# Kernel tuning notes

Measured on AMD Instinct MI355X. Metric: run time of the kernel, lower is better.

## Reference

```python
import jax, jax.numpy as jnp
import numpy as np

NUM_HEADS = 8
HEAD_DIM = 64
AVG_K_LENGTH = 20
SCALE = 1.0 / (HEAD_DIM ** 0.5 * float(np.log(AVG_K_LENGTH)))  # 1/(sqrt(dim)*log(avg_k_length))


def setup_inputs() -> dict:
    key = jax.random.key(0)
    k1, k2, k3, k4 = jax.random.split(key, 4)
    B, HD, LQ, LK = 4, NUM_HEADS * HEAD_DIM, 2048, 2048
    q = jax.random.normal(k1, (B, HD, LQ), dtype=jnp.float32)
    k = jax.random.normal(k2, (B, HD, LK), dtype=jnp.float32)
    v = jax.random.normal(k3, (B, HD, LK), dtype=jnp.float32)
    k_length = jax.random.randint(k4, (B,), 512, LK + 1, dtype=jnp.int32)
    return {"q": q, "k": k, "v": v, "k_length": k_length}


def reference(q, k, v, k_length):
    b, hd, lq = q.shape
    lk = k.shape[-1]
    d = hd // NUM_HEADS
    # b (h d) l -> b h d l
    qh = q.reshape(b, NUM_HEADS, d, lq)
    kh = k.reshape(b, NUM_HEADS, d, lk)
    vh = v.reshape(b, NUM_HEADS, d, lk)
    # per-batch entropy-invariance scale: scale * log(k_length)
    s = SCALE * jnp.log(k_length.astype(jnp.float32))[:, None, None, None]  # (b,1,1,1)
    attn = jnp.einsum('bhdq,bhdk->bhqk', qh, kh)  # (b,h,lq,lk)
    attn = jax.nn.softmax(s * attn, axis=-1)
    out = jnp.einsum('bhqk,bhdk->bhdq', attn, vh)  # (b,h,d,lq)
    return out.reshape(b, hd, lq)
```

## Files before the change

### kernel.cpp

```cpp
#include <hip/hip_runtime.h>
#include <hip/hip_bf16.h>
#include <math.h>


typedef __attribute__((ext_vector_type(8))) short short8_t;
typedef __attribute__((ext_vector_type(4))) short short4_t;
typedef __attribute__((ext_vector_type(4))) float float4_t;

#define SEQ   2048
#define NBH   32
#define NKT   32

__device__ __forceinline__ unsigned f2bf2u(float a, float b) {
#if __has_builtin(__builtin_amdgcn_cvt_pk_bf16_f32)
  typedef __bf16 bf16x2_t __attribute__((ext_vector_type(2)));
  union { bf16x2_t v; unsigned u; } cv;
  cv.v = __builtin_amdgcn_cvt_pk_bf16_f32(a, b);
  return cv.u;
#else
  union { float f; unsigned u; } x, y;
  x.f = a; y.f = b;
  unsigned ra = x.u + 0x7fffu + ((x.u >> 16) & 1u);
  unsigned rb = y.u + 0x7fffu + ((y.u >> 16) & 1u);
  return (ra >> 16) | (rb & 0xffff0000u);
#endif
}

__device__ __forceinline__ short f2bf1(float a) {
  return (short)(f2bf2u(a, a) & 0xffffu);
}

__device__ __forceinline__ float fast_exp2(float x) {
#if __has_builtin(__builtin_amdgcn_exp2f)
  return __builtin_amdgcn_exp2f(x);
#else
  return exp2f(x);
#endif
}

__device__ __forceinline__ void gld16(const void* g, void* l) {
  __builtin_amdgcn_global_load_lds(
      (const __attribute__((address_space(1))) void*)g,
      (__attribute__((address_space(3))) void*)l, 16, 0, 0);
}

__device__ __forceinline__ float4_t mfma32(short8_t a, short8_t b, float4_t c) {
  return __builtin_amdgcn_mfma_f32_16x16x32_bf16(a, b, c, 0, 0, 0);
}

__device__ __forceinline__ float4_t mfma16(short4_t a, short4_t b, float4_t c) {
#if __has_builtin(__builtin_amdgcn_mfma_f32_16x16x16bf16_1k)
  return __builtin_amdgcn_mfma_f32_16x16x16bf16_1k(a, b, c, 0, 0, 0);
#else
  asm("v_mfma_f32_16x16x16_bf16 %0, %1, %2, %0" : "+v"(c) : "v"(a), "v"(b));
  return c;
#endif
}

#define PST 68
__global__ __launch_bounds__(256, 8)
void eia_prep_kernel(const float* __restrict__ kg, const float* __restrict__ vg,
                     unsigned short* __restrict__ Kt2, unsigned short* __restrict__ Vt2) {
  __shared__ __align__(16) short T[64 * PST];
  const int id  = blockIdx.x;
  const int isV = id >> 10;
  const int sub = id & 1023;
  const int bh  = sub >> 5;
  const int kt  = sub & 31;
  const int t   = threadIdx.x;

  if (!isV) {
    const size_t ib = ((size_t)bh * 64) * SEQ + (size_t)(kt * 64) + (t & 63);
    const int dg = t >> 6;
#pragma unroll
    for (int dd = 0; dd < 16; dd += 4) {
      const int d = dg * 16 + dd;
      const float f0 = kg[ib + (size_t)(d + 0) * SEQ];
      const float f1 = kg[ib + (size_t)(d + 1) * SEQ];
      const float f2 = kg[ib + (size_t)(d + 2) * SEQ];
      const float f3 = kg[ib + (size_t)(d + 3) * SEQ];
      union { short4_t s; unsigned u[2]; } p;
      p.u[0] = f2bf2u(f0, f1);
      p.u[1] = f2bf2u(f2, f3);
      *(short4_t*)&T[(t & 63) * PST + d] = p.s;
    }
    __syncthreads();
    unsigned short* outt = Kt2 + (size_t)(bh * 32 + kt) * 4096;
#pragma unroll
    for (int rep = 0; rep < 2; ++rep) {
      const int id2 = rep * 256 + t;
      const int lr = id2 & 63, ch = id2 >> 6;
      union { short8_t v; short4_t h[2]; } o;
      o.h[0] = *(const short4_t*)&T[lr * PST + ch * 8];
      o.h[1] = *(const short4_t*)&T[lr * PST + ch * 8 + 4];
      *(short8_t*)&outt[ch * 512 + lr * 8] = o.v;
    }
  } else {
#pragma unroll
    for (int rep = 0; rep < 4; ++rep) {
      const int id2 = rep * 256 + t;
      const int d = id2 >> 4, l4 = (id2 & 15) * 4;
      const float4_t f = *(const float4_t*)&vg[((size_t)bh * 64 + d) * SEQ + kt * 64 + l4];
      union { short4_t s; unsigned u[2]; } p;
      p.u[0] = f2bf2u(f[0], f[1]);
      p.u[1] = f2bf2u(f[2], f[3]);
      *(short4_t*)&T[d * PST + l4] = p.s;
    }
    __syncthreads();
    unsigned short* outt = Vt2 + (size_t)(bh * 32 + kt) * 4096;
#pragma unroll
    for (int rep = 0; rep < 2; ++rep) {
      const int c = rep * 256 + t;
      const int k4 = c >> 5, dp = c & 31;
      union { short8_t v; short4_t h[2]; } o;
      o.h[0] = *(const short4_t*)&T[(2 * dp) * PST + k4 * 4];
      o.h[1] = *(const short4_t*)&T[(2 * dp + 1) * PST + k4 * 4];
      *(short8_t*)&outt[k4 * 256 + dp * 8] = o.v;
    }
  }
}

__global__ __launch_bounds__(256, 2)
void eia_attn_kernel(const float* __restrict__ qg,
                     const unsigned short* __restrict__ Kt2,
                     const unsigned short* __restrict__ Vt2,
                     const int* __restrict__ klen,
                     float* __restrict__ outg) {
  __shared__ __align__(16) short SM[24576];

  const int tid  = threadIdx.x;
  const int bh   = blockIdx.x & 31;
  const int qt   = blockIdx.x >> 5;
  const int q0   = qt * 128;
  const int w    = tid >> 6;
  const int lane = tid & 63;
  const int quad = lane >> 4;
  const int l16  = lane & 15;

  const float c = (1.4426950408889634f / (8.0f * 2.9957322735539909f)) *
                  logf((float)klen[bh >> 3]);
  const size_t qb = (size_t)bh * 64 * SEQ;

#pragma unroll
  for (int rep = 0; rep < 8; ++rep) {
    const int id = rep * 256 + tid;
    const int d  = id >> 5;
    const int q4 = (id & 31) * 4;
    const float4_t f = *(const float4_t*)&qg[qb + (size_t)d * SEQ + (size_t)(q0 + q4)];
    SM[(q4 + 0) * 68 + d] = f2bf1(c * f[0]);
    SM[(q4 + 1) * 68 + d] = f2bf1(c * f[1]);
    SM[(q4 + 2) * 68 + d] = f2bf1(c * f[2]);
    SM[(q4 + 3) * 68 + d] = f2bf1(c * f[3]);
  }
  __syncthreads();

  short8_t qfrag[2][2];
#pragma unroll
  for (int g = 0; g < 2; ++g)
#pragma unroll
    for (int s = 0; s < 2; ++s) {
      const short* qp = &SM[(w * 32 + g * 16 + l16) * 68 + s * 32 + quad * 8];
      const short4_t lo = *(const short4_t*)qp;
      const short4_t hi = *(const short4_t*)(qp + 4);
      qfrag[g][s] = short8_t{lo[0], lo[1], lo[2], lo[3], hi[0], hi[1], hi[2], hi[3]};
    }
  __syncthreads();

  const char* ksrc = (const char*)Kt2 + (size_t)bh * NKT * 8192 + (2 * w) * 1024 + lane * 16;
  const char* vsrc = (const char*)Vt2 + (size_t)bh * NKT * 8192 + (2 * w) * 1024 + lane * 16;
  short* const kdst = &SM[(2 * w) * 512];
  short* const vdst = &SM[12288 + (2 * w) * 512];

  const short* const kfp = &SM[quad * 512 + l16 * 8];
  const short* const vfp = &SM[12288 + quad * 256 + l16 * 4];

  const float4_t z4 = {0.f, 0.f, 0.f, 0.f};
  float4_t oacc[2][4];
#pragma unroll
  for (int g = 0; g < 2; ++g)
#pragma unroll
    for (int tt = 0; tt < 4; ++tt) oacc[g][tt] = z4;
  float4_t lacc[2] = {z4, z4};
  const short one_bf = (short)0x3F80;
  const short4_t ones4 = (l16 == 0) ? short4_t{one_bf, one_bf, one_bf, one_bf}
                                    : short4_t{0, 0, 0, 0};

  gld16(ksrc, kdst);              gld16(ksrc + 1024, kdst + 512);
  gld16(vsrc, vdst);              gld16(vsrc + 1024, vdst + 512);
  gld16(ksrc + 8192, kdst + 4096); gld16(ksrc + 8192 + 1024, kdst + 4096 + 512);
  gld16(vsrc + 8192, vdst + 4096); gld16(vsrc + 8192 + 1024, vdst + 4096 + 512);

  int  sc = 0;
  int  sn = 2;
  size_t gsrc = 2 * 8192;

  for (int kt = 0; kt < NKT; ++kt) {
    if (kt < NKT - 1) asm volatile("s_waitcnt vmcnt(4)" ::: "memory");
    else              asm volatile("s_waitcnt vmcnt(0)" ::: "memory");
    asm volatile("s_barrier" ::: "memory");

    if (kt < NKT - 2) {
      const int so = sn * 4096;
      gld16(ksrc + gsrc, kdst + so); gld16(ksrc + gsrc + 1024, kdst + so + 512);
      gld16(vsrc + gsrc, vdst + so); gld16(vsrc + gsrc + 1024, vdst + so + 512);
      gsrc += 8192;
      sn = (sn == 2) ? 0 : sn + 1;
    }
    const int koff = sc * 4096;
    sc = (sc == 2) ? 0 : sc + 1;
    const short* const kb = kfp + koff;
    const short* const vb = vfp + koff;

    float4_t sac[2][4];
#pragma unroll
    for (int t = 0; t < 4; ++t) {
      const short8_t kv = *(const short8_t*)(kb + t * 128);
      sac[0][t] = mfma32(kv, qfrag[0][0], z4);
      sac[1][t] = mfma32(kv, qfrag[1][0], z4);
    }
#pragma unroll
    for (int t = 0; t < 4; ++t) {
      const short8_t kv = *(const short8_t*)(kb + 2048 + t * 128);
      sac[0][t] = mfma32(kv, qfrag[0][1], sac[0][t]);
      sac[1][t] = mfma32(kv, qfrag[1][1], sac[1][t]);
    }

    short4_t pbf[2][4];
#pragma unroll
    for (int g = 0; g < 2; ++g)
#pragma unroll
      for (int t = 0; t < 4; ++t) {
        const float e0 = fast_exp2(sac[g][t][0]);
        const float e1 = fast_exp2(sac[g][t][1]);
        const float e2 = fast_exp2(sac[g][t][2]);
        const float e3 = fast_exp2(sac[g][t][3]);
        union { short4_t s; unsigned u[2]; } p;
        p.u[0] = f2bf2u(e0, e1);
        p.u[1] = f2bf2u(e2, e3);
        pbf[g][t] = p.s;
        lacc[g] = mfma16(ones4, pbf[g][t], lacc[g]);
      }

#pragma unroll
    for (int t = 0; t < 4; ++t) {
      const short* vfb = vb + t * 1024;
#pragma unroll
      for (int tt = 0; tt < 4; ++tt) {
        const short4_t vv = *(const short4_t*)(vfb + tt * 64);
        oacc[0][tt] = mfma16(vv, pbf[0][t], oacc[0][tt]);
        oacc[1][tt] = mfma16(vv, pbf[1][t], oacc[1][tt]);
      }
    }
  }

#pragma unroll
  for (int g = 0; g < 2; ++g) {
    const float ls  = __shfl(lacc[g][0], l16, 64);
    const float inv = 1.0f / ls;
    const size_t ob = qb + (size_t)(q0 + w * 32 + g * 16 + l16);
#pragma unroll
    for (int tt = 0; tt < 4; ++tt)
#pragma unroll
      for (int r = 0; r < 4; ++r)
        outg[ob + (size_t)(tt * 16 + quad * 4 + r) * SEQ] = oacc[g][tt][r] * inv;
  }
}

#define DPAD  72
#define PPAD  68
__global__ __launch_bounds__(256, 5)
void eia_attn_fb(const float* __restrict__ qg, const float* __restrict__ kg,
                 const float* __restrict__ vg, const int* __restrict__ klen,
                 float* __restrict__ outg) {
  __shared__ __align__(16) short QPs[64 * DPAD];
  __shared__ __align__(16) short Ksf[64 * DPAD];
  __shared__ __align__(16) short Vsf[64 * DPAD];

  const int tid  = threadIdx.x;
  const int bh   = blockIdx.x & 31;
  const int qt   = blockIdx.x >> 5;
  const int q0   = qt * 64;
  const int w    = tid >> 6;
  const int lane = tid & 63;
  const int quad = lane >> 4;
  const int l16  = lane & 15;

  const size_t base = (size_t)bh * 64 * SEQ;
  const float c = (1.4426950408889634f / (8.0f * 2.9957322735539909f)) *
                  logf((float)klen[bh >> 3]);

#pragma unroll
  for (int it = 0; it < 2; ++it) {
    const int e = it * 4 + w;
    float f[8];
#pragma unroll
    for (int j = 0; j < 8; ++j)
      f[j] = c * qg[base + (size_t)(e * 8 + j) * SEQ + (size_t)(q0 + lane)];
    union { short8_t s8; unsigned u[4]; } t;
#pragma unroll
    for (int j = 0; j < 4; ++j) t.u[j] = f2bf2u(f[2 * j], f[2 * j + 1]);
    *(short8_t*)&QPs[lane * DPAD + e * 8] = t.s8;
  }
  __syncthreads();

  short8_t qfrag[2];
#pragma unroll
  for (int s = 0; s < 2; ++s)
    qfrag[s] = *(const short8_t*)&QPs[(w * 16 + l16) * DPAD + s * 32 + quad * 8];

  float4_t oacc[4];
#pragma unroll
  for (int t = 0; t < 4; ++t) { oacc[t][0] = 0.f; oacc[t][1] = 0.f; oacc[t][2] = 0.f; oacc[t][3] = 0.f; }
  float lsumv[4] = {0.f, 0.f, 0.f, 0.f};
  const int pbase = w * (16 * DPAD);

  for (int kt = 0; kt < NKT; ++kt) {
    const int k0 = kt * 64;
#pragma unroll
    for (int it = 0; it < 2; ++it) {
      float f[8];
#pragma unroll
      for (int j = 0; j < 8; ++j)
        f[j] = kg[base + (size_t)((it * 4 + w) * 8 + j) * SEQ + (size_t)(k0 + lane)];
      union { short8_t s8; unsigned u[4]; } t;
#pragma unroll
      for (int j = 0; j < 4; ++j) t.u[j] = f2bf2u(f[2 * j], f[2 * j + 1]);
      *(short8_t*)&Ksf[lane * DPAD + (it * 4 + w) * 8] = t.s8;
    }
#pragma unroll
    for (int it = 0; it < 4; ++it) {
      const int d = it * 16 + (w << 2) + (lane >> 4);
      const float4_t vv = *(const float4_t*)&vg[base + (size_t)d * SEQ + (size_t)(k0 + ((lane & 15) << 2))];
      union { short4_t s4; unsigned u[2]; } t;
      t.u[0] = f2bf2u(vv[0], vv[1]);
      t.u[1] = f2bf2u(vv[2], vv[3]);
      *(short4_t*)&Vsf[d * DPAD + ((lane & 15) << 2)] = t.s4;
    }
    __syncthreads();

    float4_t sacc[4];
#pragma unroll
    for (int t = 0; t < 4; ++t) { sacc[t][0] = 0.f; sacc[t][1] = 0.f; sacc[t][2] = 0.f; sacc[t][3] = 0.f; }
#pragma unroll
    for (int t = 0; t < 4; ++t)
#pragma unroll
      for (int s = 0; s < 2; ++s) {
        const short8_t bf = *(const short8_t*)&Ksf[(t * 16 + l16) * DPAD + s * 32 + quad * 8];
        sacc[t] = mfma32(qfrag[s], bf, sacc[t]);
      }

#pragma unroll
    for (int r = 0; r < 4; ++r) {
      const float p0 = fast_exp2(sacc[0][r]);
      const float p1 = fast_exp2(sacc[1][r]);
      const float p2 = fast_exp2(sacc[2][r]);
      const float p3 = fast_exp2(sacc[3][r]);
      lsumv[r] += (p0 + p1) + (p2 + p3);
      const int prow = pbase + (quad * 4 + r) * PPAD + l16;
      QPs[prow +  0] = f2bf1(p0);
      QPs[prow + 16] = f2bf1(p1);
      QPs[prow + 32] = f2bf1(p2);
      QPs[prow + 48] = f2bf1(p3);
    }

#pragma unroll
    for (int s = 0; s < 2; ++s) {
      const short* pr = &QPs[pbase + l16 * PPAD + s * 32 + quad * 8];
      const short4_t plo = *(const short4_t*)pr;
      const short4_t phi = *(const short4_t*)(pr + 4);
      const short8_t pf = {plo[0], plo[1], plo[2], plo[3], phi[0], phi[1], phi[2], phi[3]};
#pragma unroll
      for (int t = 0; t < 4; ++t) {
        const short8_t vf = *(const short8_t*)&Vsf[(t * 16 + l16) * DPAD + s * 32 + quad * 8];
        oacc[t] = mfma32(pf, vf, oacc[t]);
      }
    }
    __syncthreads();
  }

  float inv[4];
#pragma unroll
  for (int r = 0; r < 4; ++r) {
    float v = lsumv[r];
    v += __shfl_xor(v, 1);
    v += __shfl_xor(v, 2);
    v += __shfl_xor(v, 4);
    v += __shfl_xor(v, 8);
    inv[r] = 1.0f / v;
  }
#pragma unroll
  for (int t = 0; t < 4; ++t)
#pragma unroll
    for (int r = 0; r < 4; ++r)
      outg[base + (size_t)(t * 16 + l16) * SEQ +
           (size_t)(q0 + w * 16 + quad * 4 + r)] = oacc[t][r] * inv[r];
}

extern "C" void kernel_launch(void* const* d_in, const int* in_sizes, int n_in,
                              void* d_out, int out_size, void* d_ws, size_t ws_size,
                              hipStream_t stream) {
  const float* q  = (const float*)d_in[0];
  const float* k  = (const float*)d_in[1];
  const float* v  = (const float*)d_in[2];
  const int*   kl = (const int*)d_in[3];
  float* out = (float*)d_out;

  const size_t TEN  = (size_t)NBH * SEQ * 64;
  const size_t need = 2 * TEN * sizeof(unsigned short);

  if (ws_size >= need) {
    unsigned short* Kt2 = (unsigned short*)d_ws;
    unsigned short* Vt2 = Kt2 + TEN;
    eia_prep_kernel<<<2048, 256, 0, stream>>>(k, v, Kt2, Vt2);
    eia_attn_kernel<<<512, 256, 0, stream>>>(q, Kt2, Vt2, kl, out);
  } else {
    eia_attn_fb<<<1024, 256, 0, stream>>>(q, k, v, kl, out);
  }
}
```

Baseline: 141.6 us.

## Split each K tile across two wave groups and reduce partial outputs via LDS

Doubles the attention block to 512 threads. Two groups of four waves each process half of every 64-key tile for the same query rows. Each group keeps its own partial output and row-sum accumulators, which are combined through shared memory at the end. This raises waves per CU and halves per-wave MFMA and exp work per tile, which should hide latency better. The cost is an extra reduction pass with two barriers, and a larger block in which one half of the waves sits idle during the final store.

After: 138.5 us. -2.2%, faster.

```diff
diff --git a/kernel.cpp b/kernel.cpp
--- a/kernel.cpp
+++ b/kernel.cpp
@@ -120,7 +120,7 @@
   }
 }
 
-__global__ __launch_bounds__(256, 2)
+__global__ __launch_bounds__(512, 4)
 void eia_attn_kernel(const float* __restrict__ qg,
                      const unsigned short* __restrict__ Kt2,
                      const unsigned short* __restrict__ Vt2,
@@ -132,7 +132,9 @@
   const int bh   = blockIdx.x & 31;
   const int qt   = blockIdx.x >> 5;
   const int q0   = qt * 128;
-  const int w    = tid >> 6;
+  const int w2   = tid >> 6;
+  const int w    = w2 & 3;
+  const int h    = w2 >> 2;
   const int lane = tid & 63;
   const int quad = lane >> 4;
   const int l16  = lane & 15;
@@ -142,8 +144,8 @@
   const size_t qb = (size_t)bh * 64 * SEQ;
 
 #pragma unroll
-  for (int rep = 0; rep < 8; ++rep) {
-    const int id = rep * 256 + tid;
+  for (int rep = 0; rep < 4; ++rep) {
+    const int id = rep * 512 + tid;
     const int d  = id >> 5;
     const int q4 = (id & 31) * 4;
     const float4_t f = *(const float4_t*)&qg[qb + (size_t)d * SEQ + (size_t)(q0 + q4)];
@@ -166,13 +168,13 @@
     }
   __syncthreads();
 
-  const char* ksrc = (const char*)Kt2 + (size_t)bh * NKT * 8192 + (2 * w) * 1024 + lane * 16;
-  const char* vsrc = (const char*)Vt2 + (size_t)bh * NKT * 8192 + (2 * w) * 1024 + lane * 16;
-  short* const kdst = &SM[(2 * w) * 512];
-  short* const vdst = &SM[12288 + (2 * w) * 512];
-
-  const short* const kfp = &SM[quad * 512 + l16 * 8];
-  const short* const vfp = &SM[12288 + quad * 256 + l16 * 4];
+  const char* ksrc = (const char*)Kt2 + (size_t)bh * NKT * 8192 + w2 * 1024 + lane * 16;
+  const char* vsrc = (const char*)Vt2 + (size_t)bh * NKT * 8192 + w2 * 1024 + lane * 16;
+  short* const kdst = &SM[w2 * 512];
+  short* const vdst = &SM[12288 + w2 * 512];
+
+  const short* const kfp = &SM[quad * 512 + l16 * 8 + h * 256];
+  const short* const vfp = &SM[12288 + quad * 256 + l16 * 4 + h * 2048];
 
   const float4_t z4 = {0.f, 0.f, 0.f, 0.f};
   float4_t oacc[2][4];
@@ -185,24 +187,23 @@
   const short4_t ones4 = (l16 == 0) ? short4_t{one_bf, one_bf, one_bf, one_bf}
                                     : short4_t{0, 0, 0, 0};
 
-  gld16(ksrc, kdst);              gld16(ksrc + 1024, kdst + 512);
-  gld16(vsrc, vdst);              gld16(vsrc + 1024, vdst + 512);
-  gld16(ksrc + 8192, kdst + 4096); gld16(ksrc + 8192 + 1024, kdst + 4096 + 512);
-  gld16(vsrc + 8192, vdst + 4096); gld16(vsrc + 8192 + 1024, vdst + 4096 + 512);
+  gld16(ksrc, kdst);               gld16(vsrc, vdst);
+  gld16(ksrc + 8192, kdst + 4096); gld16(vsrc + 8192, vdst + 4096);
+  asm volatile("s_waitcnt vmcnt(0)" ::: "memory");
 
   int  sc = 0;
   int  sn = 2;
   size_t gsrc = 2 * 8192;
 
   for (int kt = 0; kt < NKT; ++kt) {
-    if (kt < NKT - 1) asm volatile("s_waitcnt vmcnt(4)" ::: "memory");
+    if (kt < NKT - 1) asm volatile("s_waitcnt vmcnt(2)" ::: "memory");
     else              asm volatile("s_waitcnt vmcnt(0)" ::: "memory");
     asm volatile("s_barrier" ::: "memory");
 
     if (kt < NKT - 2) {
       const int so = sn * 4096;
-      gld16(ksrc + gsrc, kdst + so); gld16(ksrc + gsrc + 1024, kdst + so + 512);
-      gld16(vsrc + gsrc, vdst + so); gld16(vsrc + gsrc + 1024, vdst + so + 512);
+      gld16(ksrc + gsrc, kdst + so);
+      gld16(vsrc + gsrc, vdst + so);
       gsrc += 8192;
       sn = (sn == 2) ? 0 : sn + 1;
     }
@@ -211,58 +212,85 @@
     const short* const kb = kfp + koff;
     const short* const vb = vfp + koff;
 
-    float4_t sac[2][4];
-#pragma unroll
-    for (int t = 0; t < 4; ++t) {
-      const short8_t kv = *(const short8_t*)(kb + t * 128);
-      sac[0][t] = mfma32(kv, qfrag[0][0], z4);
-      sac[1][t] = mfma32(kv, qfrag[1][0], z4);
-    }
-#pragma unroll
-    for (int t = 0; t < 4; ++t) {
-      const short8_t kv = *(const short8_t*)(kb + 2048 + t * 128);
-      sac[0][t] = mfma32(kv, qfrag[0][1], sac[0][t]);
-      sac[1][t] = mfma32(kv, qfrag[1][1], sac[1][t]);
-    }
-
-    short4_t pbf[2][4];
+    float4_t sac[2][2];
+#pragma unroll
+    for (int tl = 0; tl < 2; ++tl) {
+      const short8_t kv = *(const short8_t*)(kb + tl * 128);
+      sac[0][tl] = mfma32(kv, qfrag[0][0], z4);
+      sac[1][tl] = mfma32(kv, qfrag[1][0], z4);
+    }
+#pragma unroll
+    for (int tl = 0; tl < 2; ++tl) {
+      const short8_t kv = *(const short8_t*)(kb + 2048 + tl * 128);
+      sac[0][tl] = mfma32(kv, qfrag[0][1], sac[0][tl]);
+      sac[1][tl] = mfma32(kv, qfrag[1][1], sac[1][tl]);
+    }
+
+    short4_t pbf[2][2];
 #pragma unroll
     for (int g = 0; g < 2; ++g)
 #pragma unroll
-      for (int t = 0; t < 4; ++t) {
-        const float e0 = fast_exp2(sac[g][t][0]);
-        const float e1 = fast_exp2(sac[g][t][1]);
-        const float e2 = fast_exp2(sac[g][t][2]);
-        const float e3 = fast_exp2(sac[g][t][3]);
+      for (int tl = 0; tl < 2; ++tl) {
+        const float e0 = fast_exp2(sac[g][tl][0]);
+        const float e1 = fast_exp2(sac[g][tl][1]);
+        const float e2 = fast_exp2(sac[g][tl][2]);
+        const float e3 = fast_exp2(sac[g][tl][3]);
         union { short4_t s; unsigned u[2]; } p;
         p.u[0] = f2bf2u(e0, e1);
         p.u[1] = f2bf2u(e2, e3);
-        pbf[g][t] = p.s;
-        lacc[g] = mfma16(ones4, pbf[g][t], lacc[g]);
+        pbf[g][tl] = p.s;
+        lacc[g] = mfma16(ones4, pbf[g][tl], lacc[g]);
       }
 
 #pragma unroll
-    for (int t = 0; t < 4; ++t) {
-      const short* vfb = vb + t * 1024;
+    for (int tl = 0; tl < 2; ++tl) {
+      const short* vfb = vb + tl * 1024;
 #pragma unroll
       for (int tt = 0; tt < 4; ++tt) {
         const short4_t vv = *(const short4_t*)(vfb + tt * 64);
-        oacc[0][tt] = mfma16(vv, pbf[0][t], oacc[0][tt]);
-        oacc[1][tt] = mfma16(vv, pbf[1][t], oacc[1][tt]);
+        oacc[0][tt] = mfma16(vv, pbf[0][tl], oacc[0][tt]);
+        oacc[1][tt] = mfma16(vv, pbf[1][tl], oacc[1][tt]);
       }
     }
   }
 
-#pragma unroll
-  for (int g = 0; g < 2; ++g) {
-    const float ls  = __shfl(lacc[g][0], l16, 64);
-    const float inv = 1.0f / ls;
-    const size_t ob = qb + (size_t)(q0 + w * 32 + g * 16 + l16);
-#pragma unroll
-    for (int tt = 0; tt < 4; ++tt)
-#pragma unroll
-      for (int r = 0; r < 4; ++r)
-        outg[ob + (size_t)(tt * 16 + quad * 4 + r) * SEQ] = oacc[g][tt][r] * inv;
+  __syncthreads();
+  float* const FA = (float*)SM;
+  float* const fb = FA + (size_t)(w * 64 + lane) * 40;
+  if (h == 1) {
+#pragma unroll
+    for (int g = 0; g < 2; ++g)
+#pragma unroll
+      for (int tt = 0; tt < 4; ++tt)
+        *(float4_t*)(fb + (g * 4 + tt) * 4) = oacc[g][tt];
+    fb[32] = lacc[0][0];
+    fb[33] = lacc[1][0];
+  }
+  __syncthreads();
+  if (h == 0) {
+#pragma unroll
+    for (int g = 0; g < 2; ++g)
+#pragma unroll
+      for (int tt = 0; tt < 4; ++tt) {
+        const float4_t o2 = *(const float4_t*)(fb + (g * 4 + tt) * 4);
+        oacc[g][tt][0] += o2[0];
+        oacc[g][tt][1] += o2[1];
+        oacc[g][tt][2] += o2[2];
+        oacc[g][tt][3] += o2[3];
+      }
+    lacc[0][0] += fb[32];
+    lacc[1][0] += fb[33];
+#pragma unroll
+    for (int g = 0; g < 2; ++g) {
+      const float ls  = __shfl(lacc[g][0], l16, 64);
+      const float inv = 1.0f / ls;
+      const size_t ob = qb + (size_t)(q0 + w * 32 + g * 16 + l16);
+#pragma unroll
+      for (int tt = 0; tt < 4; ++tt)
+#pragma unroll
+        for (int r = 0; r < 4; ++r)
+          outg[ob + (size_t)(tt * 16 + quad * 4 + r) * SEQ] = oacc[g][tt][r] * inv;
+    }
   }
 }
 
@@ -412,7 +440,7 @@
     unsigned short* Kt2 = (unsigned short*)d_ws;
     unsigned short* Vt2 = Kt2 + TEN;
     eia_prep_kernel<<<2048, 256, 0, stream>>>(k, v, Kt2, Vt2);
-    eia_attn_kernel<<<512, 256, 0, stream>>>(q, Kt2, Vt2, kl, out);
+    eia_attn_kernel<<<512, 512, 0, stream>>>(q, Kt2, Vt2, kl, out);
   } else {
     eia_attn_fb<<<1024, 256, 0, stream>>>(q, k, v, kl, out);
   }
```

## Split waves across query and key halves, load V straight to registers

Applied to the files above, without the earlier changes.

Warps are regrouped as 2 query-halves by 2 key-halves. Each warp now handles 64 queries against half of every K tile, so each K fragment read from LDS feeds four query groups instead of two. V is no longer staged in LDS: the preprocessing kernel writes V in a fragment-ready layout, and each warp loads its part directly into registers, double-buffered across an unrolled pair of iterations. Partial outputs and row sums from the two key halves are combined through LDS at the end. The cost is more registers per warp for the accumulators, a full vmcnt(0) wait every iteration, and an extra reduction step.

After: 145.8 us. +3.0%, slower.

```diff
diff --git a/kernel.cpp b/kernel.cpp
--- a/kernel.cpp
+++ b/kernel.cpp
@@ -111,11 +111,11 @@
 #pragma unroll
     for (int rep = 0; rep < 2; ++rep) {
       const int c = rep * 256 + t;
-      const int k4 = c >> 5, dp = c & 31;
+      const int kh = c >> 8, quad = (c >> 6) & 3, d = c & 63;
       union { short8_t v; short4_t h[2]; } o;
-      o.h[0] = *(const short4_t*)&T[(2 * dp) * PST + k4 * 4];
-      o.h[1] = *(const short4_t*)&T[(2 * dp + 1) * PST + k4 * 4];
-      *(short8_t*)&outt[k4 * 256 + dp * 8] = o.v;
+      o.h[0] = *(const short4_t*)&T[d * PST + kh * 32 + quad * 4];
+      o.h[1] = *(const short4_t*)&T[d * PST + kh * 32 + 16 + quad * 4];
+      *(short8_t*)&outt[c * 8] = o.v;
     }
   }
 }
@@ -126,13 +126,15 @@
                      const unsigned short* __restrict__ Vt2,
                      const int* __restrict__ klen,
                      float* __restrict__ outg) {
-  __shared__ __align__(16) short SM[24576];
+  __shared__ __align__(16) short SM[20480];
 
   const int tid  = threadIdx.x;
   const int bh   = blockIdx.x & 31;
   const int qt   = blockIdx.x >> 5;
   const int q0   = qt * 128;
-  const int w    = tid >> 6;
+  const int wv   = tid >> 6;
+  const int qh   = wv & 1;
+  const int kh   = wv >> 1;
   const int lane = tid & 63;
   const int quad = lane >> 4;
   const int l16  = lane & 15;
@@ -154,115 +156,152 @@
   }
   __syncthreads();
 
-  short8_t qfrag[2][2];
-#pragma unroll
-  for (int g = 0; g < 2; ++g)
+  short8_t qfrag[4][2];
+#pragma unroll
+  for (int g = 0; g < 4; ++g)
 #pragma unroll
     for (int s = 0; s < 2; ++s) {
-      const short* qp = &SM[(w * 32 + g * 16 + l16) * 68 + s * 32 + quad * 8];
+      const short* qp = &SM[(qh * 64 + g * 16 + l16) * 68 + s * 32 + quad * 8];
       const short4_t lo = *(const short4_t*)qp;
       const short4_t hi = *(const short4_t*)(qp + 4);
       qfrag[g][s] = short8_t{lo[0], lo[1], lo[2], lo[3], hi[0], hi[1], hi[2], hi[3]};
     }
   __syncthreads();
 
-  const char* ksrc = (const char*)Kt2 + (size_t)bh * NKT * 8192 + (2 * w) * 1024 + lane * 16;
-  const char* vsrc = (const char*)Vt2 + (size_t)bh * NKT * 8192 + (2 * w) * 1024 + lane * 16;
-  short* const kdst = &SM[(2 * w) * 512];
-  short* const vdst = &SM[12288 + (2 * w) * 512];
-
+  const char* ksrc = (const char*)Kt2 + (size_t)bh * NKT * 8192 + (2 * wv) * 1024 + lane * 16;
+  short* const kdst = &SM[(2 * wv) * 512];
   const short* const kfp = &SM[quad * 512 + l16 * 8];
-  const short* const vfp = &SM[12288 + quad * 256 + l16 * 4];
+
+  const char* const vgl = (const char*)Vt2 + (size_t)bh * NKT * 8192 +
+                          kh * 4096 + quad * 1024 + l16 * 16;
 
   const float4_t z4 = {0.f, 0.f, 0.f, 0.f};
-  float4_t oacc[2][4];
-#pragma unroll
-  for (int g = 0; g < 2; ++g)
+  float4_t oacc[4][4];
+#pragma unroll
+  for (int g = 0; g < 4; ++g)
 #pragma unroll
     for (int tt = 0; tt < 4; ++tt) oacc[g][tt] = z4;
-  float4_t lacc[2] = {z4, z4};
+  float4_t lacc[4] = {z4, z4, z4, z4};
   const short one_bf = (short)0x3F80;
   const short4_t ones4 = (l16 == 0) ? short4_t{one_bf, one_bf, one_bf, one_bf}
                                     : short4_t{0, 0, 0, 0};
 
-  gld16(ksrc, kdst);              gld16(ksrc + 1024, kdst + 512);
-  gld16(vsrc, vdst);              gld16(vsrc + 1024, vdst + 512);
+  union vfrag { short8_t v; short4_t h[2]; };
+  vfrag vA[4], vB[4];
+
+  gld16(ksrc, kdst);               gld16(ksrc + 1024, kdst + 512);
   gld16(ksrc + 8192, kdst + 4096); gld16(ksrc + 8192 + 1024, kdst + 4096 + 512);
-  gld16(vsrc + 8192, vdst + 4096); gld16(vsrc + 8192 + 1024, vdst + 4096 + 512);
+#pragma unroll
+  for (int tt = 0; tt < 4; ++tt)
+    vA[tt].v = *(const short8_t*)(vgl + tt * 256);
 
   int  sc = 0;
   int  sn = 2;
   size_t gsrc = 2 * 8192;
 
-  for (int kt = 0; kt < NKT; ++kt) {
-    if (kt < NKT - 1) asm volatile("s_waitcnt vmcnt(4)" ::: "memory");
-    else              asm volatile("s_waitcnt vmcnt(0)" ::: "memory");
-    asm volatile("s_barrier" ::: "memory");
-
-    if (kt < NKT - 2) {
-      const int so = sn * 4096;
-      gld16(ksrc + gsrc, kdst + so); gld16(ksrc + gsrc + 1024, kdst + so + 512);
-      gld16(vsrc + gsrc, vdst + so); gld16(vsrc + gsrc + 1024, vdst + so + 512);
-      gsrc += 8192;
-      sn = (sn == 2) ? 0 : sn + 1;
-    }
-    const int koff = sc * 4096;
-    sc = (sc == 2) ? 0 : sc + 1;
-    const short* const kb = kfp + koff;
-    const short* const vb = vfp + koff;
-
-    float4_t sac[2][4];
-#pragma unroll
-    for (int t = 0; t < 4; ++t) {
-      const short8_t kv = *(const short8_t*)(kb + t * 128);
-      sac[0][t] = mfma32(kv, qfrag[0][0], z4);
-      sac[1][t] = mfma32(kv, qfrag[1][0], z4);
-    }
-#pragma unroll
-    for (int t = 0; t < 4; ++t) {
-      const short8_t kv = *(const short8_t*)(kb + 2048 + t * 128);
-      sac[0][t] = mfma32(kv, qfrag[0][1], sac[0][t]);
-      sac[1][t] = mfma32(kv, qfrag[1][1], sac[1][t]);
-    }
-
-    short4_t pbf[2][4];
-#pragma unroll
-    for (int g = 0; g < 2; ++g)
-#pragma unroll
-      for (int t = 0; t < 4; ++t) {
-        const float e0 = fast_exp2(sac[g][t][0]);
-        const float e1 = fast_exp2(sac[g][t][1]);
-        const float e2 = fast_exp2(sac[g][t][2]);
-        const float e3 = fast_exp2(sac[g][t][3]);
-        union { short4_t s; unsigned u[2]; } p;
-        p.u[0] = f2bf2u(e0, e1);
-        p.u[1] = f2bf2u(e2, e3);
-        pbf[g][t] = p.s;
-        lacc[g] = mfma16(ones4, pbf[g][t], lacc[g]);
+#define EIA_BODY(KT, VC, VN)                                                  \
+  do {                                                                        \
+    asm volatile("s_waitcnt vmcnt(0)" ::: "memory");                          \
+    asm volatile("s_barrier" ::: "memory");                                   \
+    if ((KT) < NKT - 2) {                                                     \
+      const int so = sn * 4096;                                               \
+      gld16(ksrc + gsrc, kdst + so);                                          \
+      gld16(ksrc + gsrc + 1024, kdst + so + 512);                             \
+      gsrc += 8192;                                                           \
+      sn = (sn == 2) ? 0 : sn + 1;                                            \
+    }                                                                         \
+    if ((KT) < NKT - 1) {                                                     \
+      const char* vp = vgl + (size_t)((KT) + 1) * 8192;                       \
+      _Pragma("unroll")                                                       \
+      for (int tt = 0; tt < 4; ++tt)                                          \
+        VN[tt].v = *(const short8_t*)(vp + tt * 256);                         \
+    }                                                                         \
+    const int koff = sc * 4096;                                               \
+    sc = (sc == 2) ? 0 : sc + 1;                                              \
+    const short* const kb = kfp + koff;                                       \
+             \
+    float4_t sac[4][2];                                                       \
+    _Pragma("unroll")                                                         \
+    for (int tl = 0; tl < 2; ++tl) {                                          \
+      const short8_t kv = *(const short8_t*)(kb + (kh * 2 + tl) * 128);       \
+      _Pragma("unroll")                                                       \
+      for (int g = 0; g < 4; ++g) sac[g][tl] = mfma32(kv, qfrag[g][0], z4);   \
+    }                                                                         \
+    _Pragma("unroll")                                                         \
+    for (int tl = 0; tl < 2; ++tl) {                                          \
+      const short8_t kv = *(const short8_t*)(kb + 2048 + (kh * 2 + tl) * 128);\
+      _Pragma("unroll")                                                       \
+      for (int g = 0; g < 4; ++g)                                             \
+        sac[g][tl] = mfma32(kv, qfrag[g][1], sac[g][tl]);                     \
+    }                                                                         \
+              \
+    short4_t pbf[4][2];                                                       \
+    _Pragma("unroll")                                                         \
+    for (int g = 0; g < 4; ++g)                                               \
+      _Pragma("unroll")                                                       \
+      for (int tl = 0; tl < 2; ++tl) {                                        \
+        const float e0 = fast_exp2(sac[g][tl][0]);                            \
+        const float e1 = fast_exp2(sac[g][tl][1]);                            \
+        const float e2 = fast_exp2(sac[g][tl][2]);                            \
+        const float e3 = fast_exp2(sac[g][tl][3]);                            \
+        union { short4_t s; unsigned u[2]; } p;                               \
+        p.u[0] = f2bf2u(e0, e1);                                              \
+        p.u[1] = f2bf2u(e2, e3);                                              \
+        pbf[g][tl] = p.s;                                                     \
+        lacc[g] = mfma16(ones4, pbf[g][tl], lacc[g]);                         \
+      }                                                                       \
+                                \
+    _Pragma("unroll")                                                         \
+    for (int tt = 0; tt < 4; ++tt)                                            \
+      _Pragma("unroll")                                                       \
+      for (int tl = 0; tl < 2; ++tl) {                                        \
+        const short4_t vv = VC[tt].h[tl];                                     \
+        _Pragma("unroll")                                                     \
+        for (int g = 0; g < 4; ++g)                                           \
+          oacc[g][tt] = mfma16(vv, pbf[g][tl], oacc[g][tt]);                  \
+      }                                                                       \
+  } while (0)
+
+  for (int kt = 0; kt < NKT; kt += 2) {
+    EIA_BODY(kt,     vA, vB);
+    EIA_BODY(kt + 1, vB, vA);
+  }
+#undef EIA_BODY
+
+  __syncthreads();
+  float* const FA = (float*)SM;
+  float* const fb = FA + (size_t)(qh * 64 + lane) * 68;
+  if (kh == 1) {
+#pragma unroll
+    for (int g = 0; g < 4; ++g)
+#pragma unroll
+      for (int tt = 0; tt < 4; ++tt)
+        *(float4_t*)(fb + (g * 4 + tt) * 4) = oacc[g][tt];
+#pragma unroll
+    for (int g = 0; g < 4; ++g) fb[64 + g] = lacc[g][0];
+  }
+  __syncthreads();
+  if (kh == 0) {
+#pragma unroll
+    for (int g = 0; g < 4; ++g) {
+#pragma unroll
+      for (int tt = 0; tt < 4; ++tt) {
+        const float4_t o2 = *(const float4_t*)(fb + (g * 4 + tt) * 4);
+        oacc[g][tt][0] += o2[0];
+        oacc[g][tt][1] += o2[1];
+        oacc[g][tt][2] += o2[2];
+        oacc[g][tt][3] += o2[3];
       }
-
-#pragma unroll
-    for (int t = 0; t < 4; ++t) {
-      const short* vfb = vb + t * 1024;
-#pragma unroll
-      for (int tt = 0; tt < 4; ++tt) {
-        const short4_t vv = *(const short4_t*)(vfb + tt * 64);
-        oacc[0][tt] = mfma16(vv, pbf[0][t], oacc[0][tt]);
-        oacc[1][tt] = mfma16(vv, pbf[1][t], oacc[1][tt]);
-      }
-    }
-  }
-
-#pragma unroll
-  for (int g = 0; g < 2; ++g) {
-    const float ls  = __shfl(lacc[g][0], l16, 64);
-    const float inv = 1.0f / ls;
-    const size_t ob = qb + (size_t)(q0 + w * 32 + g * 16 + l16);
-#pragma unroll
-    for (int tt = 0; tt < 4; ++tt)
-#pragma unroll
-      for (int r = 0; r < 4; ++r)
-        outg[ob + (size_t)(tt * 16 + quad * 4 + r) * SEQ] = oacc[g][tt][r] * inv;
+      const float lsp = lacc[g][0] + fb[64 + g];
+      const float ls  = __shfl(lsp, l16, 64);
+      const float inv = 1.0f / ls;
+      const size_t ob = qb + (size_t)(q0 + qh * 64 + g * 16 + l16);
+#pragma unroll
+      for (int tt = 0; tt < 4; ++tt)
+#pragma unroll
+        for (int r = 0; r < 4; ++r)
+          outg[ob + (size_t)(tt * 16 + quad * 4 + r) * SEQ] = oacc[g][tt][r] * inv;
+    }
   }
 }
 
```

## Switch attention kernel to 32x32x16 MFMA with permlane32 swap for P

Applied to the files above, without the earlier changes.

Replaces the 16x16 MFMA tiling in the main attention kernel with 32x32x16 bf16 MFMAs for both QK^T and PV. Each wave now handles 32 query rows. The softmax probabilities are rearranged into the B-operand layout with permlane32_swap instead of going through LDS. The row sum is computed with VALU adds and a single cross-half shuffle rather than a ones-vector MFMA, and the V prep kernel writes a new layout to match. The aim is fewer MFMA issues and less per-tile overhead. It adds an extra vmcnt(0) wait in the prologue and depends on the permlane32 builtin, with a shuffle fallback.

Result: no change. 139.8 us (-1.3%).

```diff
diff --git a/kernel.cpp b/kernel.cpp
--- a/kernel.cpp
+++ b/kernel.cpp
@@ -6,6 +6,7 @@
 typedef __attribute__((ext_vector_type(8))) short short8_t;
 typedef __attribute__((ext_vector_type(4))) short short4_t;
 typedef __attribute__((ext_vector_type(4))) float float4_t;
+typedef __attribute__((ext_vector_type(16))) float float16_t;
 
 #define SEQ   2048
 #define NBH   32
@@ -48,12 +49,21 @@
   return __builtin_amdgcn_mfma_f32_16x16x32_bf16(a, b, c, 0, 0, 0);
 }
 
-__device__ __forceinline__ float4_t mfma16(short4_t a, short4_t b, float4_t c) {
-#if __has_builtin(__builtin_amdgcn_mfma_f32_16x16x16bf16_1k)
-  return __builtin_amdgcn_mfma_f32_16x16x16bf16_1k(a, b, c, 0, 0, 0);
+__device__ __forceinline__ float16_t mfma3232(short8_t a, short8_t b, float16_t c) {
+  return __builtin_amdgcn_mfma_f32_32x32x16_bf16(a, b, c, 0, 0, 0);
+}
+
+__device__ __forceinline__ void plswap(unsigned& a, unsigned& b, int hi) {
+#if __has_builtin(__builtin_amdgcn_permlane32_swap)
+  typedef __attribute__((ext_vector_type(2))) unsigned uint2_t;
+  uint2_t r = __builtin_amdgcn_permlane32_swap(a, b, false, false);
+  a = r[0]; b = r[1];
 #else
-  asm("v_mfma_f32_16x16x16_bf16 %0, %1, %2, %0" : "+v"(c) : "v"(a), "v"(b));
-  return c;
+  const unsigned sa = (unsigned)__shfl_xor((int)a, 32);
+  const unsigned sb = (unsigned)__shfl_xor((int)b, 32);
+  const unsigned an = hi ? sb : a;
+  const unsigned bn = hi ? b : sa;
+  a = an; b = bn;
 #endif
 }
 
@@ -111,11 +121,11 @@
 #pragma unroll
     for (int rep = 0; rep < 2; ++rep) {
       const int c = rep * 256 + t;
-      const int k4 = c >> 5, dp = c & 31;
+      const int kc = c >> 6, d = c & 63;
       union { short8_t v; short4_t h[2]; } o;
-      o.h[0] = *(const short4_t*)&T[(2 * dp) * PST + k4 * 4];
-      o.h[1] = *(const short4_t*)&T[(2 * dp + 1) * PST + k4 * 4];
-      *(short8_t*)&outt[k4 * 256 + dp * 8] = o.v;
+      o.h[0] = *(const short4_t*)&T[d * PST + kc * 8];
+      o.h[1] = *(const short4_t*)&T[d * PST + kc * 8 + 4];
+      *(short8_t*)&outt[c * 8] = o.v;
     }
   }
 }
@@ -128,14 +138,14 @@
                      float* __restrict__ outg) {
   __shared__ __align__(16) short SM[24576];
 
-  const int tid  = threadIdx.x;
-  const int bh   = blockIdx.x & 31;
-  const int qt   = blockIdx.x >> 5;
-  const int q0   = qt * 128;
-  const int w    = tid >> 6;
-  const int lane = tid & 63;
-  const int quad = lane >> 4;
-  const int l16  = lane & 15;
+  const int tid   = threadIdx.x;
+  const int bh    = blockIdx.x & 31;
+  const int qt    = blockIdx.x >> 5;
+  const int q0    = qt * 128;
+  const int qw    = tid >> 6;
+  const int lane  = tid & 63;
+  const int l31   = lane & 31;
+  const int hi    = lane >> 5;
 
   const float c = (1.4426950408889634f / (8.0f * 2.9957322735539909f)) *
                   logf((float)klen[bh >> 3]);
@@ -154,41 +164,33 @@
   }
   __syncthreads();
 
-  short8_t qfrag[2][2];
-#pragma unroll
-  for (int g = 0; g < 2; ++g)
-#pragma unroll
-    for (int s = 0; s < 2; ++s) {
-      const short* qp = &SM[(w * 32 + g * 16 + l16) * 68 + s * 32 + quad * 8];
-      const short4_t lo = *(const short4_t*)qp;
-      const short4_t hi = *(const short4_t*)(qp + 4);
-      qfrag[g][s] = short8_t{lo[0], lo[1], lo[2], lo[3], hi[0], hi[1], hi[2], hi[3]};
-    }
+  short8_t qfrag[4];
+#pragma unroll
+  for (int s = 0; s < 4; ++s) {
+    const short* qp = &SM[(qw * 32 + l31) * 68 + s * 16 + hi * 8];
+    const short4_t lo = *(const short4_t*)qp;
+    const short4_t hh = *(const short4_t*)(qp + 4);
+    qfrag[s] = short8_t{lo[0], lo[1], lo[2], lo[3], hh[0], hh[1], hh[2], hh[3]};
+  }
   __syncthreads();
 
-  const char* ksrc = (const char*)Kt2 + (size_t)bh * NKT * 8192 + (2 * w) * 1024 + lane * 16;
-  const char* vsrc = (const char*)Vt2 + (size_t)bh * NKT * 8192 + (2 * w) * 1024 + lane * 16;
-  short* const kdst = &SM[(2 * w) * 512];
-  short* const vdst = &SM[12288 + (2 * w) * 512];
-
-  const short* const kfp = &SM[quad * 512 + l16 * 8];
-  const short* const vfp = &SM[12288 + quad * 256 + l16 * 4];
-
-  const float4_t z4 = {0.f, 0.f, 0.f, 0.f};
-  float4_t oacc[2][4];
-#pragma unroll
-  for (int g = 0; g < 2; ++g)
-#pragma unroll
-    for (int tt = 0; tt < 4; ++tt) oacc[g][tt] = z4;
-  float4_t lacc[2] = {z4, z4};
-  const short one_bf = (short)0x3F80;
-  const short4_t ones4 = (l16 == 0) ? short4_t{one_bf, one_bf, one_bf, one_bf}
-                                    : short4_t{0, 0, 0, 0};
-
-  gld16(ksrc, kdst);              gld16(ksrc + 1024, kdst + 512);
-  gld16(vsrc, vdst);              gld16(vsrc + 1024, vdst + 512);
+  const char* ksrc = (const char*)Kt2 + (size_t)bh * NKT * 8192 + (2 * qw) * 1024 + lane * 16;
+  const char* vsrc = (const char*)Vt2 + (size_t)bh * NKT * 8192 + (2 * qw) * 1024 + lane * 16;
+  short* const kdst = &SM[(2 * qw) * 512];
+  short* const vdst = &SM[12288 + (2 * qw) * 512];
+
+  const int lofs = hi * 512 + l31 * 8;
+
+  const float16_t z16 = {0.f,0.f,0.f,0.f,0.f,0.f,0.f,0.f,
+                         0.f,0.f,0.f,0.f,0.f,0.f,0.f,0.f};
+  float16_t oacc0 = z16, oacc1 = z16;
+  float ls = 0.f;
+
+  gld16(ksrc, kdst);               gld16(ksrc + 1024, kdst + 512);
+  gld16(vsrc, vdst);               gld16(vsrc + 1024, vdst + 512);
   gld16(ksrc + 8192, kdst + 4096); gld16(ksrc + 8192 + 1024, kdst + 4096 + 512);
   gld16(vsrc + 8192, vdst + 4096); gld16(vsrc + 8192 + 1024, vdst + 4096 + 512);
+  asm volatile("s_waitcnt vmcnt(0)" ::: "memory");
 
   int  sc = 0;
   int  sn = 2;
@@ -208,61 +210,59 @@
     }
     const int koff = sc * 4096;
     sc = (sc == 2) ? 0 : sc + 1;
-    const short* const kb = kfp + koff;
-    const short* const vb = vfp + koff;
-
-    float4_t sac[2][4];
-#pragma unroll
-    for (int t = 0; t < 4; ++t) {
-      const short8_t kv = *(const short8_t*)(kb + t * 128);
-      sac[0][t] = mfma32(kv, qfrag[0][0], z4);
-      sac[1][t] = mfma32(kv, qfrag[1][0], z4);
-    }
-#pragma unroll
-    for (int t = 0; t < 4; ++t) {
-      const short8_t kv = *(const short8_t*)(kb + 2048 + t * 128);
-      sac[0][t] = mfma32(kv, qfrag[0][1], sac[0][t]);
-      sac[1][t] = mfma32(kv, qfrag[1][1], sac[1][t]);
-    }
-
-    short4_t pbf[2][4];
-#pragma unroll
-    for (int g = 0; g < 2; ++g)
-#pragma unroll
-      for (int t = 0; t < 4; ++t) {
-        const float e0 = fast_exp2(sac[g][t][0]);
-        const float e1 = fast_exp2(sac[g][t][1]);
-        const float e2 = fast_exp2(sac[g][t][2]);
-        const float e3 = fast_exp2(sac[g][t][3]);
-        union { short4_t s; unsigned u[2]; } p;
-        p.u[0] = f2bf2u(e0, e1);
-        p.u[1] = f2bf2u(e2, e3);
-        pbf[g][t] = p.s;
-        lacc[g] = mfma16(ones4, pbf[g][t], lacc[g]);
+    const short* const kb_ = &SM[koff + lofs];
+    const short* const vb_ = &SM[12288 + koff + lofs];
+
+    float16_t s0 = z16, s1 = z16;
+#pragma unroll
+    for (int s = 0; s < 4; ++s)
+      s0 = mfma3232(*(const short8_t*)(kb_ + s * 1024), qfrag[s], s0);
+#pragma unroll
+    for (int s = 0; s < 4; ++s)
+      s1 = mfma3232(*(const short8_t*)(kb_ + 256 + s * 1024), qfrag[s], s1);
+
+    union pfu { short8_t s8; unsigned u[4]; };
+    pfu pf[4];
+#pragma unroll
+    for (int kb = 0; kb < 2; ++kb) {
+      float e[16];
+#pragma unroll
+      for (int r = 0; r < 16; ++r)
+        e[r] = fast_exp2(kb == 0 ? s0[r] : s1[r]);
+      ls += (((e[0] + e[1]) + (e[2] + e[3])) + ((e[4] + e[5]) + (e[6] + e[7]))) +
+            (((e[8] + e[9]) + (e[10] + e[11])) + ((e[12] + e[13]) + (e[14] + e[15])));
+#pragma unroll
+      for (int ksl = 0; ksl < 2; ++ksl) {
+        const int b = ksl * 8;
+        unsigned a02 = f2bf2u(e[b + 0], e[b + 1]);
+        unsigned b02 = f2bf2u(e[b + 4], e[b + 5]);
+        unsigned a13 = f2bf2u(e[b + 2], e[b + 3]);
+        unsigned b13 = f2bf2u(e[b + 6], e[b + 7]);
+        plswap(a02, b02, hi);
+        plswap(a13, b13, hi);
+        pf[kb * 2 + ksl].u[0] = a02;
+        pf[kb * 2 + ksl].u[1] = a13;
+        pf[kb * 2 + ksl].u[2] = b02;
+        pf[kb * 2 + ksl].u[3] = b13;
       }
-
-#pragma unroll
-    for (int t = 0; t < 4; ++t) {
-      const short* vfb = vb + t * 1024;
-#pragma unroll
-      for (int tt = 0; tt < 4; ++tt) {
-        const short4_t vv = *(const short4_t*)(vfb + tt * 64);
-        oacc[0][tt] = mfma16(vv, pbf[0][t], oacc[0][tt]);
-        oacc[1][tt] = mfma16(vv, pbf[1][t], oacc[1][tt]);
-      }
-    }
-  }
-
-#pragma unroll
-  for (int g = 0; g < 2; ++g) {
-    const float ls  = __shfl(lacc[g][0], l16, 64);
-    const float inv = 1.0f / ls;
-    const size_t ob = qb + (size_t)(q0 + w * 32 + g * 16 + l16);
-#pragma unroll
-    for (int tt = 0; tt < 4; ++tt)
-#pragma unroll
-      for (int r = 0; r < 4; ++r)
-        outg[ob + (size_t)(tt * 16 + quad * 4 + r) * SEQ] = oacc[g][tt][r] * inv;
+    }
+
+#pragma unroll
+    for (int ks = 0; ks < 4; ++ks)
+      oacc0 = mfma3232(*(const short8_t*)(vb_ + ks * 1024), pf[ks].s8, oacc0);
+#pragma unroll
+    for (int ks = 0; ks < 4; ++ks)
+      oacc1 = mfma3232(*(const short8_t*)(vb_ + 256 + ks * 1024), pf[ks].s8, oacc1);
+  }
+
+  const float lst = ls + __shfl_xor(ls, 32);
+  const float inv = 1.0f / lst;
+  const size_t ob = qb + (size_t)(q0 + qw * 32 + l31);
+#pragma unroll
+  for (int r = 0; r < 16; ++r) {
+    const int drow = (r & 3) + 8 * (r >> 2) + 4 * hi;
+    outg[ob + (size_t)(drow) * SEQ]      = oacc0[r] * inv;
+    outg[ob + (size_t)(drow + 32) * SEQ] = oacc1[r] * inv;
   }
 }
 
@@ -368,11 +368,11 @@
       const short* pr = &QPs[pbase + l16 * PPAD + s * 32 + quad * 8];
       const short4_t plo = *(const short4_t*)pr;
       const short4_t phi = *(const short4_t*)(pr + 4);
-      const short8_t pf = {plo[0], plo[1], plo[2], plo[3], phi[0], phi[1], phi[2], phi[3]};
+      const short8_t pfv = {plo[0], plo[1], plo[2], plo[3], phi[0], phi[1], phi[2], phi[3]};
 #pragma unroll
       for (int t = 0; t < 4; ++t) {
         const short8_t vf = *(const short8_t*)&Vsf[(t * 16 + l16) * DPAD + s * 32 + quad * 8];
-        oacc[t] = mfma32(pf, vf, oacc[t]);
+        oacc[t] = mfma32(pfv, vf, oacc[t]);
       }
     }
     __syncthreads();
```
